# Performance work log

Measured on AMD Instinct MI355X. Metric: run time of the kernel, lower is better.

Reference implementation:

```python
import jax, jax.numpy as jnp
import numpy as np

N, E = 100000, 1600000
DIN, DH, DOUT = 128, 64, 4


def setup_inputs() -> dict:
    key = jax.random.key(0)
    ks = jax.random.split(key, 16)
    dims = [(DIN, DH), (DH, DH), (DH, DH), (DH, DH), (DH, DH), (DH, DOUT)]
    inp = {
        "x": jax.random.normal(ks[0], (N, DIN), dtype=jnp.float32),
        "edge_index": jax.random.randint(ks[1], (2, E), 0, N, dtype=jnp.int32),
    }
    for i, (di, do) in enumerate(dims):
        scale = 1.0 / np.sqrt(di)
        inp[f"W{i}"] = jax.random.normal(ks[2 + i], (di, do), dtype=jnp.float32) * scale
        inp[f"b{i}"] = jnp.zeros((do,), dtype=jnp.float32)
    return inp


def _gcn_graph(edge_index, n):
    # PyG gcn_norm with self-loops: D^{-1/2} (A+I) D^{-1/2}
    loops = jnp.arange(n, dtype=edge_index.dtype)
    src = jnp.concatenate([edge_index[0], loops])  # message sources
    dst = jnp.concatenate([edge_index[1], loops])  # aggregation targets
    deg = jax.ops.segment_sum(jnp.ones(src.shape[0], jnp.float32), dst, num_segments=n)
    dinv = jnp.where(deg > 0, jax.lax.rsqrt(deg), 0.0)
    norm = dinv[src] * dinv[dst]  # [E+N]
    return src, dst, norm


def _gcn_layer(x, src, dst, norm, W, b, n):
    h = x @ W                                   # [N, dout] dense transform first (PyG order)
    msg = h[src] * norm[:, None]                # gather + scale, [E+N, dout]
    return jax.ops.segment_sum(msg, dst, num_segments=n) + b


def reference(x, edge_index, W0, b0, W1, b1, W2, b2, W3, b3, W4, b4, W5, b5):
    n = x.shape[0]
    src, dst, norm = _gcn_graph(edge_index, n)
    Ws = [W0, W1, W2, W3, W4, W5]
    bs = [b0, b1, b2, b3, b4, b5]
    for i in range(len(Ws)):
        x = _gcn_layer(x, src, dst, norm, Ws[i], bs[i], n)
        if i < len(Ws) - 1:
            # eval mode: dropout / edge_dropout are identity
            x = jnp.where(x >= 0, x, 0.2 * x)  # leaky_relu, negative_slope=0.2
    return x
```

## Files before the change

kernel.cpp:

```cpp
#include <hip/hip_runtime.h>


__device__ __forceinline__ float readlane_f(float v, int l) {
    union { float f; int i; } u;
    u.f = v;
    u.i = __builtin_amdgcn_readlane(u.i, l);
    return u.f;
}

__global__ __launch_bounds__(256) void bucket_hist(const int* __restrict__ dst,
                                                   int* __restrict__ ghist,
                                                   int E, int NB) {
    __shared__ int h[1024];
    for (int i = threadIdx.x; i < NB; i += 256) h[i] = 0;
    __syncthreads();
    int i = blockIdx.x * blockDim.x + threadIdx.x;
    int stride = gridDim.x * blockDim.x;
    for (; i < E; i += stride) atomicAdd(&h[dst[i] >> 7], 1);
    __syncthreads();
    for (int j = threadIdx.x; j < NB; j += 256) {
        int c = h[j];
        if (c) atomicAdd(&ghist[j], c);
    }
}

__global__ void bucket_scan(const int* __restrict__ ghist, int* __restrict__ base,
                            int* __restrict__ cursor, int NB, int E) {
    int tid = threadIdx.x, lane = tid & 63, wid = tid >> 6;
    int v = (tid < NB) ? ghist[tid] : 0;
    int incl = v;
#pragma unroll
    for (int off = 1; off < 64; off <<= 1) {
        int t = __shfl_up(incl, off);
        if (lane >= off) incl += t;
    }
    __shared__ int ws[16];
    if (lane == 63) ws[wid] = incl;
    __syncthreads();
    if (tid == 0) {
        int run = 0;
        for (int i = 0; i < 16; ++i) { int t = ws[i]; ws[i] = run; run += t; }
    }
    __syncthreads();
    int excl = ws[wid] + incl - v;
    if (tid < NB) { base[tid] = excl; cursor[tid] = excl; }
    if (tid == 0) base[NB] = E;
}

__global__ __launch_bounds__(256) void bucket_scatter(
    const int* __restrict__ src, const int* __restrict__ dst,
    int* __restrict__ cursor, int* __restrict__ bsrc,
    unsigned char* __restrict__ bdl, int E, int NB) {
    __shared__ int h[1024];
    __shared__ int rb[1024];
    const int CH = 4096;
    for (int c0 = blockIdx.x * CH; c0 < E; c0 += gridDim.x * CH) {
        int cend = c0 + CH < E ? c0 + CH : E;
        for (int j = threadIdx.x; j < NB; j += 256) h[j] = 0;
        __syncthreads();
        for (int i = c0 + threadIdx.x; i < cend; i += 256)
            atomicAdd(&h[dst[i] >> 7], 1);
        __syncthreads();
        for (int j = threadIdx.x; j < NB; j += 256) {
            int c = h[j];
            rb[j] = c ? atomicAdd(&cursor[j], c) : 0;
            h[j] = 0;
        }
        __syncthreads();
        for (int i = c0 + threadIdx.x; i < cend; i += 256) {
            int d = dst[i];
            int b = d >> 7;
            int p = rb[b] + atomicAdd(&h[b], 1);
            bsrc[p] = src[i];
            bdl[p] = (unsigned char)(d & 127);
        }
        __syncthreads();
    }
}

__global__ __launch_bounds__(256) void bucket_finalize(
    const int* __restrict__ base, const int* __restrict__ bsrc,
    const unsigned char* __restrict__ bdl, int* __restrict__ rowptr,
    int* __restrict__ ssrc, float* __restrict__ dinv, int N, int NB, int E) {
    __shared__ int cnt[128];
    __shared__ int cur[128];
    __shared__ int w0sum;
    const int tid = threadIdx.x;
    const int lane = tid & 63;
    for (int b = blockIdx.x; b < NB; b += gridDim.x) {
        const int s = base[b], e = base[b + 1];
        const int d0 = b << 7;
        const int w = (N - d0 < 128) ? (N - d0) : 128;
        if (tid < 128) cnt[tid] = 0;
        __syncthreads();
        for (int i = s + tid; i < e; i += 256) atomicAdd(&cnt[bdl[i]], 1);
        __syncthreads();
        int v = (tid < 128) ? cnt[tid] : 0;
        int incl = v;
#pragma unroll
        for (int off = 1; off < 64; off <<= 1) {
            int t = __shfl_up(incl, off);
            if (lane >= off) incl += t;
        }
        if (tid == 63) w0sum = incl;
        __syncthreads();
        int excl = incl - v + ((tid >= 64 && tid < 128) ? w0sum : 0);
        if (tid < 128) cur[tid] = s + excl;
        if (tid < w) {
            rowptr[d0 + tid] = s + excl;
            dinv[d0 + tid] = rsqrtf((float)(v + 1));
        }
        __syncthreads();
        for (int i = s + tid; i < e; i += 256) {
            int p = atomicAdd(&cur[bdl[i]], 1);
            ssrc[p] = bsrc[i];
        }
        __syncthreads();
    }
    if (blockIdx.x == 0 && tid == 0) rowptr[N] = E;
}

template <int K, bool LRELU>
__global__ __launch_bounds__(256) void gemm_h(
    const float* __restrict__ x, const float* __restrict__ W,
    float* __restrict__ h, int n) {
    const int lane = threadIdx.x & 63;
    const int gw = blockIdx.x * (blockDim.x >> 6) + (threadIdx.x >> 6);
    const int nw = gridDim.x * (blockDim.x >> 6);

    float wreg[K];
#pragma unroll
    for (int k = 0; k < K; ++k) wreg[k] = W[k * 64 + lane];

    for (int row = gw; row < n; row += nw) {
        float xv0 = x[(size_t)row * K + lane];
        if (LRELU) xv0 = xv0 >= 0.f ? xv0 : 0.2f * xv0;
        float xv1 = 0.f;
        if (K == 128) {
            xv1 = x[(size_t)row * K + 64 + lane];
            if (LRELU) xv1 = xv1 >= 0.f ? xv1 : 0.2f * xv1;
        }
        float a0 = 0.f, a1 = 0.f, a2 = 0.f, a3 = 0.f;
#pragma unroll
        for (int k = 0; k < 64; k += 4) {
            a0 = fmaf(readlane_f(xv0, k + 0), wreg[k + 0], a0);
            a1 = fmaf(readlane_f(xv0, k + 1), wreg[k + 1], a1);
            a2 = fmaf(readlane_f(xv0, k + 2), wreg[k + 2], a2);
            a3 = fmaf(readlane_f(xv0, k + 3), wreg[k + 3], a3);
        }
        if (K == 128) {
#pragma unroll
            for (int k = 0; k < 64; k += 4) {
                a0 = fmaf(readlane_f(xv1, k + 0), wreg[64 + k + 0], a0);
                a1 = fmaf(readlane_f(xv1, k + 1), wreg[64 + k + 1], a1);
                a2 = fmaf(readlane_f(xv1, k + 2), wreg[64 + k + 2], a2);
                a3 = fmaf(readlane_f(xv1, k + 3), wreg[64 + k + 3], a3);
            }
        }
        h[(size_t)row * 64 + lane] = (a0 + a1) + (a2 + a3);
    }
}

__global__ __launch_bounds__(256) void csr_agg64(
    const float* __restrict__ h, const int* __restrict__ rowptr,
    const int* __restrict__ ssrc, const float* __restrict__ dinv,
    const float* __restrict__ b, float* __restrict__ agg, int n) {
    const int lane = threadIdx.x & 63;
    int w = blockIdx.x * (blockDim.x >> 6) + (threadIdx.x >> 6);
    const int nw = gridDim.x * (blockDim.x >> 6);
    const float bl = b[lane];
    for (int d = w; d < n; d += nw) {
        const float di = dinv[d];
        float acc = fmaf(di * di, h[(size_t)d * 64 + lane], bl);
        int e = rowptr[d], end = rowptr[d + 1];
        for (; e + 4 <= end; e += 4) {
            int s0 = ssrc[e], s1 = ssrc[e + 1], s2 = ssrc[e + 2], s3 = ssrc[e + 3];
            float n0 = di * dinv[s0], n1 = di * dinv[s1];
            float n2 = di * dinv[s2], n3 = di * dinv[s3];
            float v0 = h[(size_t)s0 * 64 + lane], v1 = h[(size_t)s1 * 64 + lane];
            float v2 = h[(size_t)s2 * 64 + lane], v3 = h[(size_t)s3 * 64 + lane];
            acc = fmaf(v0, n0, acc);
            acc = fmaf(v1, n1, acc);
            acc = fmaf(v2, n2, acc);
            acc = fmaf(v3, n3, acc);
        }
        for (; e < end; ++e) {
            int s = ssrc[e];
            acc = fmaf(h[(size_t)s * 64 + lane], di * dinv[s], acc);
        }
        agg[(size_t)d * 64 + lane] = acc;
    }
}

__global__ __launch_bounds__(256) void gemm4_h(
    const float* __restrict__ x, const float* __restrict__ W,
    float* __restrict__ h4, int n) {
    int i = blockIdx.x * blockDim.x + threadIdx.x;
    int stride = gridDim.x * blockDim.x;
    for (; i < n; i += stride) {
        const float4* xr = (const float4*)(x + (size_t)i * 64);
        float a0 = 0.f, a1 = 0.f, a2 = 0.f, a3 = 0.f;
#pragma unroll
        for (int k4 = 0; k4 < 16; ++k4) {
            float4 xv = xr[k4];
            float e0 = xv.x >= 0.f ? xv.x : 0.2f * xv.x;
            float e1 = xv.y >= 0.f ? xv.y : 0.2f * xv.y;
            float e2 = xv.z >= 0.f ? xv.z : 0.2f * xv.z;
            float e3 = xv.w >= 0.f ? xv.w : 0.2f * xv.w;
            int k = k4 * 4;
            a0 = fmaf(e0, W[(k + 0) * 4 + 0], a0); a1 = fmaf(e0, W[(k + 0) * 4 + 1], a1);
            a2 = fmaf(e0, W[(k + 0) * 4 + 2], a2); a3 = fmaf(e0, W[(k + 0) * 4 + 3], a3);
            a0 = fmaf(e1, W[(k + 1) * 4 + 0], a0); a1 = fmaf(e1, W[(k + 1) * 4 + 1], a1);
            a2 = fmaf(e1, W[(k + 1) * 4 + 2], a2); a3 = fmaf(e1, W[(k + 1) * 4 + 3], a3);
            a0 = fmaf(e2, W[(k + 2) * 4 + 0], a0); a1 = fmaf(e2, W[(k + 2) * 4 + 1], a1);
            a2 = fmaf(e2, W[(k + 2) * 4 + 2], a2); a3 = fmaf(e2, W[(k + 2) * 4 + 3], a3);
            a0 = fmaf(e3, W[(k + 3) * 4 + 0], a0); a1 = fmaf(e3, W[(k + 3) * 4 + 1], a1);
            a2 = fmaf(e3, W[(k + 3) * 4 + 2], a2); a3 = fmaf(e3, W[(k + 3) * 4 + 3], a3);
        }
        ((float4*)h4)[i] = make_float4(a0, a1, a2, a3);
    }
}

__global__ __launch_bounds__(256) void csr_agg4(
    const float* __restrict__ h4, const int* __restrict__ rowptr,
    const int* __restrict__ ssrc, const float* __restrict__ dinv,
    const float* __restrict__ b, float* __restrict__ out, int n) {
    int i = blockIdx.x * blockDim.x + threadIdx.x;
    int stride = gridDim.x * blockDim.x;
    float b0 = b[0], b1 = b[1], b2 = b[2], b3 = b[3];
    for (; i < n; i += stride) {
        float di = dinv[i];
        float d2 = di * di;
        float4 hv = ((const float4*)h4)[i];
        float a0 = fmaf(d2, hv.x, b0), a1 = fmaf(d2, hv.y, b1);
        float a2 = fmaf(d2, hv.z, b2), a3 = fmaf(d2, hv.w, b3);
        int e = rowptr[i], end = rowptr[i + 1];
        for (; e < end; ++e) {
            int s = ssrc[e];
            float nrm = di * dinv[s];
            float4 v = ((const float4*)h4)[s];
            a0 = fmaf(nrm, v.x, a0); a1 = fmaf(nrm, v.y, a1);
            a2 = fmaf(nrm, v.z, a2); a3 = fmaf(nrm, v.w, a3);
        }
        ((float4*)out)[i] = make_float4(a0, a1, a2, a3);
    }
}

static inline size_t al64(size_t x) { return (x + 63) & ~(size_t)63; }

extern "C" void kernel_launch(void* const* d_in, const int* in_sizes, int n_in,
                              void* d_out, int out_size, void* d_ws, size_t ws_size,
                              hipStream_t stream) {
    const float* x  = (const float*)d_in[0];
    const int* ei   = (const int*)d_in[1];
    const float* W0 = (const float*)d_in[2];
    const float* b0 = (const float*)d_in[3];
    const float* W1 = (const float*)d_in[4];
    const float* b1 = (const float*)d_in[5];
    const float* W2 = (const float*)d_in[6];
    const float* b2 = (const float*)d_in[7];
    const float* W3 = (const float*)d_in[8];
    const float* b3 = (const float*)d_in[9];
    const float* W4 = (const float*)d_in[10];
    const float* b4 = (const float*)d_in[11];
    const float* W5 = (const float*)d_in[12];
    const float* b5 = (const float*)d_in[13];

    const int N = in_sizes[0] / 128;
    const int E = in_sizes[1] / 2;
    const int* src  = ei;
    const int* dstp = ei + E;
    const int NB = (N + 127) >> 7;

    float* ws = (float*)d_ws;
    size_t off = 0;
    int*   rowptr = (int*)(ws + off);   off += al64((size_t)N + 1);
    float* dinv   = ws + off;           off += al64((size_t)N);
    int*   ssrc   = (int*)(ws + off);   off += al64((size_t)E);
    float* bufA   = ws + off;           off += (size_t)64 * N;
    float* bufB   = ws + off;

    int* ghist = (int*)bufA;
    int* bbase = ghist + 1024;
    int* bcur  = bbase + 1088;
    int* bsrc  = (int*)(bufA + 4096);
    unsigned char* bdl = (unsigned char*)(bsrc + E);

    hipMemsetAsync(ghist, 0, 1024 * sizeof(int), stream);
    bucket_hist<<<391, 256, 0, stream>>>(dstp, ghist, E, NB);
    bucket_scan<<<1, 1024, 0, stream>>>(ghist, bbase, bcur, NB, E);
    bucket_scatter<<<391, 256, 0, stream>>>(src, dstp, bcur, bsrc, bdl, E, NB);
    bucket_finalize<<<NB, 256, 0, stream>>>(bbase, bsrc, bdl, rowptr, ssrc, dinv, N, NB, E);

    gemm_h<128, false><<<2048, 256, 0, stream>>>(x, W0, bufA, N);
    csr_agg64<<<2048, 256, 0, stream>>>(bufA, rowptr, ssrc, dinv, b0, bufB, N);

    const float* Ws[4] = {W1, W2, W3, W4};
    const float* bs[4] = {b1, b2, b3, b4};
    for (int l = 0; l < 4; ++l) {
        gemm_h<64, true><<<2048, 256, 0, stream>>>(bufB, Ws[l], bufA, N);
        csr_agg64<<<2048, 256, 0, stream>>>(bufA, rowptr, ssrc, dinv, bs[l], bufB, N);
    }

    gemm4_h<<<1024, 256, 0, stream>>>(bufB, W5, bufA, N);
    csr_agg4<<<2048, 256, 0, stream>>>(bufA, rowptr, ssrc, dinv, b5, (float*)d_out, N);
}
```

Measured before the change: 599.8 us.

## Store hidden features in 8-wide feature slices to shrink gather working set

Result: slower. 1.377 ms (+129.5%).

```diff
diff --git a/kernel.cpp b/kernel.cpp
--- a/kernel.cpp
+++ b/kernel.cpp
@@ -120,26 +120,30 @@
     if (blockIdx.x == 0 && tid == 0) rowptr[N] = E;
 }
 
-template <int K, bool LRELU>
+template <int K, bool LRELU, bool IN_SLICED>
 __global__ __launch_bounds__(256) void gemm_h(
     const float* __restrict__ x, const float* __restrict__ W,
-    float* __restrict__ h, int n) {
+    float* __restrict__ hS, int n) {
     const int lane = threadIdx.x & 63;
     const int gw = blockIdx.x * (blockDim.x >> 6) + (threadIdx.x >> 6);
     const int nw = gridDim.x * (blockDim.x >> 6);
+    const int sl = lane >> 3, f8 = lane & 7;
+    const int slot = sl * n * 8 + f8;
 
     float wreg[K];
 #pragma unroll
     for (int k = 0; k < K; ++k) wreg[k] = W[k * 64 + lane];
 
     for (int row = gw; row < n; row += nw) {
-        float xv0 = x[(size_t)row * K + lane];
+        float xv0, xv1 = 0.f;
+        if (IN_SLICED) {
+            xv0 = __builtin_nontemporal_load(x + (size_t)slot + (size_t)row * 8);
+        } else {
+            xv0 = __builtin_nontemporal_load(x + (size_t)row * K + lane);
+            if (K == 128)
+                xv1 = __builtin_nontemporal_load(x + (size_t)row * K + 64 + lane);
+        }
         if (LRELU) xv0 = xv0 >= 0.f ? xv0 : 0.2f * xv0;
-        float xv1 = 0.f;
-        if (K == 128) {
-            xv1 = x[(size_t)row * K + 64 + lane];
-            if (LRELU) xv1 = xv1 >= 0.f ? xv1 : 0.2f * xv1;
-        }
         float a0 = 0.f, a1 = 0.f, a2 = 0.f, a3 = 0.f;
 #pragma unroll
         for (int k = 0; k < 64; k += 4) {
@@ -157,57 +161,71 @@
                 a3 = fmaf(readlane_f(xv1, k + 3), wreg[64 + k + 3], a3);
             }
         }
-        h[(size_t)row * 64 + lane] = (a0 + a1) + (a2 + a3);
-    }
-}
-
-__global__ __launch_bounds__(256) void csr_agg64(
-    const float* __restrict__ h, const int* __restrict__ rowptr,
+        float acc = (a0 + a1) + (a2 + a3);
+        __builtin_nontemporal_store(acc, hS + (size_t)slot + (size_t)row * 8);
+    }
+}
+
+__global__ __launch_bounds__(256) void csr_agg_sliced(
+    const float* __restrict__ hS, const int* __restrict__ rowptr,
     const int* __restrict__ ssrc, const float* __restrict__ dinv,
-    const float* __restrict__ b, float* __restrict__ agg, int n) {
-    const int lane = threadIdx.x & 63;
-    int w = blockIdx.x * (blockDim.x >> 6) + (threadIdx.x >> 6);
-    const int nw = gridDim.x * (blockDim.x >> 6);
-    const float bl = b[lane];
-    for (int d = w; d < n; d += nw) {
+    const float* __restrict__ b, float* __restrict__ aggS, int N) {
+    const int s = blockIdx.x & 7;
+    const int cb = blockIdx.x >> 3;
+    const int nchunk = gridDim.x >> 3;
+    const int g = threadIdx.x >> 3;
+    const int f = threadIdx.x & 7;
+    const float* __restrict__ h = hS + (size_t)s * N * 8;
+    float* __restrict__ agg = aggS + (size_t)s * N * 8;
+    const float bf = b[s * 8 + f];
+
+    for (int d = cb * 32 + g; d < N; d += nchunk * 32) {
         const float di = dinv[d];
-        float acc = fmaf(di * di, h[(size_t)d * 64 + lane], bl);
-        int e = rowptr[d], end = rowptr[d + 1];
+        float acc = fmaf(di * di, h[d * 8 + f], bf);
+        int e = rowptr[d];
+        const int end = rowptr[d + 1];
         for (; e + 4 <= end; e += 4) {
-            int s0 = ssrc[e], s1 = ssrc[e + 1], s2 = ssrc[e + 2], s3 = ssrc[e + 3];
+            int s0 = __builtin_nontemporal_load(ssrc + e);
+            int s1 = __builtin_nontemporal_load(ssrc + e + 1);
+            int s2 = __builtin_nontemporal_load(ssrc + e + 2);
+            int s3 = __builtin_nontemporal_load(ssrc + e + 3);
             float n0 = di * dinv[s0], n1 = di * dinv[s1];
             float n2 = di * dinv[s2], n3 = di * dinv[s3];
-            float v0 = h[(size_t)s0 * 64 + lane], v1 = h[(size_t)s1 * 64 + lane];
-            float v2 = h[(size_t)s2 * 64 + lane], v3 = h[(size_t)s3 * 64 + lane];
+            float v0 = h[s0 * 8 + f], v1 = h[s1 * 8 + f];
+            float v2 = h[s2 * 8 + f], v3 = h[s3 * 8 + f];
             acc = fmaf(v0, n0, acc);
             acc = fmaf(v1, n1, acc);
             acc = fmaf(v2, n2, acc);
             acc = fmaf(v3, n3, acc);
         }
         for (; e < end; ++e) {
-            int s = ssrc[e];
-            acc = fmaf(h[(size_t)s * 64 + lane], di * dinv[s], acc);
-        }
-        agg[(size_t)d * 64 + lane] = acc;
+            int s0 = __builtin_nontemporal_load(ssrc + e);
+            acc = fmaf(h[s0 * 8 + f], di * dinv[s0], acc);
+        }
+        __builtin_nontemporal_store(acc, agg + d * 8 + f);
     }
 }
 
 __global__ __launch_bounds__(256) void gemm4_h(
-    const float* __restrict__ x, const float* __restrict__ W,
+    const float* __restrict__ xS, const float* __restrict__ W,
     float* __restrict__ h4, int n) {
     int i = blockIdx.x * blockDim.x + threadIdx.x;
     int stride = gridDim.x * blockDim.x;
     for (; i < n; i += stride) {
-        const float4* xr = (const float4*)(x + (size_t)i * 64);
         float a0 = 0.f, a1 = 0.f, a2 = 0.f, a3 = 0.f;
 #pragma unroll
-        for (int k4 = 0; k4 < 16; ++k4) {
-            float4 xv = xr[k4];
-            float e0 = xv.x >= 0.f ? xv.x : 0.2f * xv.x;
-            float e1 = xv.y >= 0.f ? xv.y : 0.2f * xv.y;
-            float e2 = xv.z >= 0.f ? xv.z : 0.2f * xv.z;
-            float e3 = xv.w >= 0.f ? xv.w : 0.2f * xv.w;
-            int k = k4 * 4;
+        for (int s = 0; s < 8; ++s) {
+            const float4* p = (const float4*)(xS + (size_t)s * n * 8 + (size_t)i * 8);
+            float4 u = p[0], v = p[1];
+            float e0 = u.x >= 0.f ? u.x : 0.2f * u.x;
+            float e1 = u.y >= 0.f ? u.y : 0.2f * u.y;
+            float e2 = u.z >= 0.f ? u.z : 0.2f * u.z;
+            float e3 = u.w >= 0.f ? u.w : 0.2f * u.w;
+            float e4 = v.x >= 0.f ? v.x : 0.2f * v.x;
+            float e5 = v.y >= 0.f ? v.y : 0.2f * v.y;
+            float e6 = v.z >= 0.f ? v.z : 0.2f * v.z;
+            float e7 = v.w >= 0.f ? v.w : 0.2f * v.w;
+            int k = s * 8;
             a0 = fmaf(e0, W[(k + 0) * 4 + 0], a0); a1 = fmaf(e0, W[(k + 0) * 4 + 1], a1);
             a2 = fmaf(e0, W[(k + 0) * 4 + 2], a2); a3 = fmaf(e0, W[(k + 0) * 4 + 3], a3);
             a0 = fmaf(e1, W[(k + 1) * 4 + 0], a0); a1 = fmaf(e1, W[(k + 1) * 4 + 1], a1);
@@ -216,6 +234,14 @@
             a2 = fmaf(e2, W[(k + 2) * 4 + 2], a2); a3 = fmaf(e2, W[(k + 2) * 4 + 3], a3);
             a0 = fmaf(e3, W[(k + 3) * 4 + 0], a0); a1 = fmaf(e3, W[(k + 3) * 4 + 1], a1);
             a2 = fmaf(e3, W[(k + 3) * 4 + 2], a2); a3 = fmaf(e3, W[(k + 3) * 4 + 3], a3);
+            a0 = fmaf(e4, W[(k + 4) * 4 + 0], a0); a1 = fmaf(e4, W[(k + 4) * 4 + 1], a1);
+            a2 = fmaf(e4, W[(k + 4) * 4 + 2], a2); a3 = fmaf(e4, W[(k + 4) * 4 + 3], a3);
+            a0 = fmaf(e5, W[(k + 5) * 4 + 0], a0); a1 = fmaf(e5, W[(k + 5) * 4 + 1], a1);
+            a2 = fmaf(e5, W[(k + 5) * 4 + 2], a2); a3 = fmaf(e5, W[(k + 5) * 4 + 3], a3);
+            a0 = fmaf(e6, W[(k + 6) * 4 + 0], a0); a1 = fmaf(e6, W[(k + 6) * 4 + 1], a1);
+            a2 = fmaf(e6, W[(k + 6) * 4 + 2], a2); a3 = fmaf(e6, W[(k + 6) * 4 + 3], a3);
+            a0 = fmaf(e7, W[(k + 7) * 4 + 0], a0); a1 = fmaf(e7, W[(k + 7) * 4 + 1], a1);
+            a2 = fmaf(e7, W[(k + 7) * 4 + 2], a2); a3 = fmaf(e7, W[(k + 7) * 4 + 3], a3);
         }
         ((float4*)h4)[i] = make_float4(a0, a1, a2, a3);
     }
@@ -236,7 +262,7 @@
         float a2 = fmaf(d2, hv.z, b2), a3 = fmaf(d2, hv.w, b3);
         int e = rowptr[i], end = rowptr[i + 1];
         for (; e < end; ++e) {
-            int s = ssrc[e];
+            int s = __builtin_nontemporal_load(ssrc + e);
             float nrm = di * dinv[s];
             float4 v = ((const float4*)h4)[s];
             a0 = fmaf(nrm, v.x, a0); a1 = fmaf(nrm, v.y, a1);
@@ -292,14 +318,14 @@
     bucket_scatter<<<391, 256, 0, stream>>>(src, dstp, bcur, bsrc, bdl, E, NB);
     bucket_finalize<<<NB, 256, 0, stream>>>(bbase, bsrc, bdl, rowptr, ssrc, dinv, N, NB, E);
 
-    gemm_h<128, false><<<2048, 256, 0, stream>>>(x, W0, bufA, N);
-    csr_agg64<<<2048, 256, 0, stream>>>(bufA, rowptr, ssrc, dinv, b0, bufB, N);
+    gemm_h<128, false, false><<<2048, 256, 0, stream>>>(x, W0, bufA, N);
+    csr_agg_sliced<<<2048, 256, 0, stream>>>(bufA, rowptr, ssrc, dinv, b0, bufB, N);
 
     const float* Ws[4] = {W1, W2, W3, W4};
     const float* bs[4] = {b1, b2, b3, b4};
     for (int l = 0; l < 4; ++l) {
-        gemm_h<64, true><<<2048, 256, 0, stream>>>(bufB, Ws[l], bufA, N);
-        csr_agg64<<<2048, 256, 0, stream>>>(bufA, rowptr, ssrc, dinv, bs[l], bufB, N);
+        gemm_h<64, true, true><<<2048, 256, 0, stream>>>(bufB, Ws[l], bufA, N);
+        csr_agg_sliced<<<2048, 256, 0, stream>>>(bufA, rowptr, ssrc, dinv, bs[l], bufB, N);
     }
 
     gemm4_h<<<1024, 256, 0, stream>>>(bufB, W5, bufA, N);
```

## Prescale features by dinv and balance CSR aggregation by edge count

Applied to the files above, without the earlier changes.

Measured after the change: 613.7 us. +2.3%, slower.

```diff
diff --git a/kernel.cpp b/kernel.cpp
--- a/kernel.cpp
+++ b/kernel.cpp
@@ -121,9 +121,9 @@
 }
 
 template <int K, bool LRELU>
-__global__ __launch_bounds__(256) void gemm_h(
-    const float* __restrict__ x, const float* __restrict__ W,
-    float* __restrict__ h, int n) {
+__global__ __launch_bounds__(256) void gemm_hs(
+    const float* __restrict__ in, const float* __restrict__ W,
+    const float* __restrict__ dinv, float* __restrict__ hs, int n) {
     const int lane = threadIdx.x & 63;
     const int gw = blockIdx.x * (blockDim.x >> 6) + (threadIdx.x >> 6);
     const int nw = gridDim.x * (blockDim.x >> 6);
@@ -133,13 +133,10 @@
     for (int k = 0; k < K; ++k) wreg[k] = W[k * 64 + lane];
 
     for (int row = gw; row < n; row += nw) {
-        float xv0 = x[(size_t)row * K + lane];
+        float xv0 = in[(size_t)row * K + lane];
         if (LRELU) xv0 = xv0 >= 0.f ? xv0 : 0.2f * xv0;
         float xv1 = 0.f;
-        if (K == 128) {
-            xv1 = x[(size_t)row * K + 64 + lane];
-            if (LRELU) xv1 = xv1 >= 0.f ? xv1 : 0.2f * xv1;
-        }
+        if (K == 128) xv1 = in[(size_t)row * K + 64 + lane];
         float a0 = 0.f, a1 = 0.f, a2 = 0.f, a3 = 0.f;
 #pragma unroll
         for (int k = 0; k < 64; k += 4) {
@@ -157,48 +154,72 @@
                 a3 = fmaf(readlane_f(xv1, k + 3), wreg[64 + k + 3], a3);
             }
         }
-        h[(size_t)row * 64 + lane] = (a0 + a1) + (a2 + a3);
-    }
-}
-
-__global__ __launch_bounds__(256) void csr_agg64(
-    const float* __restrict__ h, const int* __restrict__ rowptr,
+        float acc = (a0 + a1) + (a2 + a3);
+        hs[(size_t)row * 64 + lane] = dinv[row] * acc;
+    }
+}
+
+__global__ __launch_bounds__(256) void csr_agg_stream(
+    const float* __restrict__ hs, const int* __restrict__ rowptr,
     const int* __restrict__ ssrc, const float* __restrict__ dinv,
-    const float* __restrict__ b, float* __restrict__ agg, int n) {
+    const float* __restrict__ b, float* __restrict__ y,
+    int N, int E, int nwaves) {
     const int lane = threadIdx.x & 63;
-    int w = blockIdx.x * (blockDim.x >> 6) + (threadIdx.x >> 6);
-    const int nw = gridDim.x * (blockDim.x >> 6);
+    const int w = blockIdx.x * (blockDim.x >> 6) + (threadIdx.x >> 6);
+    if (w >= nwaves) return;
     const float bl = b[lane];
-    for (int d = w; d < n; d += nw) {
-        const float di = dinv[d];
-        float acc = fmaf(di * di, h[(size_t)d * 64 + lane], bl);
-        int e = rowptr[d], end = rowptr[d + 1];
-        for (; e + 4 <= end; e += 4) {
-            int s0 = ssrc[e], s1 = ssrc[e + 1], s2 = ssrc[e + 2], s3 = ssrc[e + 3];
-            float n0 = di * dinv[s0], n1 = di * dinv[s1];
-            float n2 = di * dinv[s2], n3 = di * dinv[s3];
-            float v0 = h[(size_t)s0 * 64 + lane], v1 = h[(size_t)s1 * 64 + lane];
-            float v2 = h[(size_t)s2 * 64 + lane], v3 = h[(size_t)s3 * 64 + lane];
-            acc = fmaf(v0, n0, acc);
-            acc = fmaf(v1, n1, acc);
-            acc = fmaf(v2, n2, acc);
-            acc = fmaf(v3, n3, acc);
+
+    auto lb = [&](long long t) {
+        int lo = 0, hi = N;
+        while (lo < hi) {
+            int m = (lo + hi) >> 1;
+            if ((long long)rowptr[m] < t) lo = m + 1; else hi = m;
+        }
+        return lo;
+    };
+    const long long q0 = (long long)w * E / nwaves;
+    const long long q1 = (long long)(w + 1) * E / nwaves;
+    int r0 = lb(q0);
+    int r1 = (w == nwaves - 1) ? N : lb(q1);
+
+    for (int d = r0; d < r1; ++d) {
+        int e = __builtin_amdgcn_readfirstlane(rowptr[d]);
+        const int end = __builtin_amdgcn_readfirstlane(rowptr[d + 1]);
+        float acc0 = hs[(size_t)d * 64 + lane];
+        float acc1 = 0.f;
+        for (; e + 8 <= end; e += 8) {
+            int s0 = ssrc[e + 0], s1 = ssrc[e + 1];
+            int s2 = ssrc[e + 2], s3 = ssrc[e + 3];
+            int s4 = ssrc[e + 4], s5 = ssrc[e + 5];
+            int s6 = ssrc[e + 6], s7 = ssrc[e + 7];
+            float v0 = hs[(size_t)s0 * 64 + lane];
+            float v1 = hs[(size_t)s1 * 64 + lane];
+            float v2 = hs[(size_t)s2 * 64 + lane];
+            float v3 = hs[(size_t)s3 * 64 + lane];
+            float v4 = hs[(size_t)s4 * 64 + lane];
+            float v5 = hs[(size_t)s5 * 64 + lane];
+            float v6 = hs[(size_t)s6 * 64 + lane];
+            float v7 = hs[(size_t)s7 * 64 + lane];
+            acc0 += v0 + v2;
+            acc1 += v1 + v3;
+            acc0 += v4 + v6;
+            acc1 += v5 + v7;
         }
         for (; e < end; ++e) {
             int s = ssrc[e];
-            acc = fmaf(h[(size_t)s * 64 + lane], di * dinv[s], acc);
-        }
-        agg[(size_t)d * 64 + lane] = acc;
-    }
-}
-
-__global__ __launch_bounds__(256) void gemm4_h(
-    const float* __restrict__ x, const float* __restrict__ W,
-    float* __restrict__ h4, int n) {
+            acc0 += hs[(size_t)s * 64 + lane];
+        }
+        y[(size_t)d * 64 + lane] = fmaf(dinv[d], acc0 + acc1, bl);
+    }
+}
+
+__global__ __launch_bounds__(256) void gemm4_hs(
+    const float* __restrict__ y, const float* __restrict__ W,
+    const float* __restrict__ dinv, float* __restrict__ hs4, int n) {
     int i = blockIdx.x * blockDim.x + threadIdx.x;
     int stride = gridDim.x * blockDim.x;
     for (; i < n; i += stride) {
-        const float4* xr = (const float4*)(x + (size_t)i * 64);
+        const float4* xr = (const float4*)(y + (size_t)i * 64);
         float a0 = 0.f, a1 = 0.f, a2 = 0.f, a3 = 0.f;
 #pragma unroll
         for (int k4 = 0; k4 < 16; ++k4) {
@@ -217,32 +238,30 @@
             a0 = fmaf(e3, W[(k + 3) * 4 + 0], a0); a1 = fmaf(e3, W[(k + 3) * 4 + 1], a1);
             a2 = fmaf(e3, W[(k + 3) * 4 + 2], a2); a3 = fmaf(e3, W[(k + 3) * 4 + 3], a3);
         }
-        ((float4*)h4)[i] = make_float4(a0, a1, a2, a3);
+        float di = dinv[i];
+        ((float4*)hs4)[i] = make_float4(di * a0, di * a1, di * a2, di * a3);
     }
 }
 
 __global__ __launch_bounds__(256) void csr_agg4(
-    const float* __restrict__ h4, const int* __restrict__ rowptr,
+    const float* __restrict__ hs4, const int* __restrict__ rowptr,
     const int* __restrict__ ssrc, const float* __restrict__ dinv,
     const float* __restrict__ b, float* __restrict__ out, int n) {
     int i = blockIdx.x * blockDim.x + threadIdx.x;
     int stride = gridDim.x * blockDim.x;
     float b0 = b[0], b1 = b[1], b2 = b[2], b3 = b[3];
     for (; i < n; i += stride) {
-        float di = dinv[i];
-        float d2 = di * di;
-        float4 hv = ((const float4*)h4)[i];
-        float a0 = fmaf(d2, hv.x, b0), a1 = fmaf(d2, hv.y, b1);
-        float a2 = fmaf(d2, hv.z, b2), a3 = fmaf(d2, hv.w, b3);
+        float4 hv = ((const float4*)hs4)[i];
+        float a0 = hv.x, a1 = hv.y, a2 = hv.z, a3 = hv.w;
         int e = rowptr[i], end = rowptr[i + 1];
         for (; e < end; ++e) {
             int s = ssrc[e];
-            float nrm = di * dinv[s];
-            float4 v = ((const float4*)h4)[s];
-            a0 = fmaf(nrm, v.x, a0); a1 = fmaf(nrm, v.y, a1);
-            a2 = fmaf(nrm, v.z, a2); a3 = fmaf(nrm, v.w, a3);
-        }
-        ((float4*)out)[i] = make_float4(a0, a1, a2, a3);
+            float4 v = ((const float4*)hs4)[s];
+            a0 += v.x; a1 += v.y; a2 += v.z; a3 += v.w;
+        }
+        float di = dinv[i];
+        ((float4*)out)[i] = make_float4(fmaf(di, a0, b0), fmaf(di, a1, b1),
+                                        fmaf(di, a2, b2), fmaf(di, a3, b3));
     }
 }
 
@@ -292,16 +311,19 @@
     bucket_scatter<<<391, 256, 0, stream>>>(src, dstp, bcur, bsrc, bdl, E, NB);
     bucket_finalize<<<NB, 256, 0, stream>>>(bbase, bsrc, bdl, rowptr, ssrc, dinv, N, NB, E);
 
-    gemm_h<128, false><<<2048, 256, 0, stream>>>(x, W0, bufA, N);
-    csr_agg64<<<2048, 256, 0, stream>>>(bufA, rowptr, ssrc, dinv, b0, bufB, N);
+    const int AGG_BLOCKS = 2048;
+    const int NWAVES = AGG_BLOCKS * 4;
+
+    gemm_hs<128, false><<<2048, 256, 0, stream>>>(x, W0, dinv, bufA, N);
+    csr_agg_stream<<<AGG_BLOCKS, 256, 0, stream>>>(bufA, rowptr, ssrc, dinv, b0, bufB, N, E, NWAVES);
 
     const float* Ws[4] = {W1, W2, W3, W4};
     const float* bs[4] = {b1, b2, b3, b4};
     for (int l = 0; l < 4; ++l) {
-        gemm_h<64, true><<<2048, 256, 0, stream>>>(bufB, Ws[l], bufA, N);
-        csr_agg64<<<2048, 256, 0, stream>>>(bufA, rowptr, ssrc, dinv, bs[l], bufB, N);
-    }
-
-    gemm4_h<<<1024, 256, 0, stream>>>(bufB, W5, bufA, N);
-    csr_agg4<<<2048, 256, 0, stream>>>(bufA, rowptr, ssrc, dinv, b5, (float*)d_out, N);
-}
+        gemm_hs<64, true><<<2048, 256, 0, stream>>>(bufB, Ws[l], dinv, bufA, N);
+        csr_agg_stream<<<AGG_BLOCKS, 256, 0, stream>>>(bufA, rowptr, ssrc, dinv, bs[l], bufB, N, E, NWAVES);
+    }
+
+    gemm4_hs<<<1024, 256, 0, stream>>>(bufB, W5, dinv, bufA, N);
+    csr_agg4<<<512, 256, 0, stream>>>(bufA, rowptr, ssrc, dinv, b5, (float*)d_out, N);
+}
```
